# Performance work log

Hardware: AMD Instinct MI355X
Metric: run time of the kernel (lower is better)

## Reference

```python
import jax, jax.numpy as jnp
import numpy as np

B, N, H, HID, LOCALITY = 2, 4096, 4, 256, 30.0
VD = HID // H
F32_MAX = jnp.finfo(jnp.float32).max


def setup_inputs() -> dict:
    key = jax.random.key(0)
    k1, k2, k3, k4 = jax.random.split(key, 4)
    m_dist = jax.random.uniform(k1, (B, N, N), dtype=jnp.float32)  # pairwise distances (b,N,N)
    x = jax.random.normal(k2, (B, N, HID), dtype=jnp.float32)
    r = jax.random.normal(k3, (1, H, 1, 1), dtype=jnp.float32)  # learned per-head distance scale
    # lecun_normal: std = 1/sqrt(fan_in), fan_in = HID
    weight = jax.random.normal(k4, (H, HID, VD), dtype=jnp.float32) / np.sqrt(HID)
    return {"m_dist": m_dist, "x": x, "r": r, "weight": weight}


def reference(m_dist, x, r, weight):
    # scaled distance per head: (b,h,n,n)
    scaled = m_dist[:, None, :, :] * (r ** 2)
    # percentile-thresholded local mask (linear interpolation, per row)
    thresh = jnp.percentile(scaled, LOCALITY, axis=-1, keepdims=True, method="linear")
    scaled = jnp.where(scaled <= thresh, scaled, F32_MAX)
    att = jax.nn.softmax(-scaled, axis=-1)  # (b,h,n,n)
    value = jnp.einsum("bnj,hjk->bhnk", x, weight)  # (b,h,n,v)
    out = jnp.einsum("bhnj,bhjd->bhnd", att, value)  # (b,h,n,v)
    out = jnp.transpose(out, (0, 2, 1, 3)).reshape(out.shape[0], -1, HID)  # (b,n,hid)
    return jax.nn.gelu(out, approximate=False)
```

## Files before the change

kernel.cpp:

```cpp
#include <hip/hip_runtime.h>
#include <hip/hip_bf16.h>

#define Bc   2
#define Nc   4096
#define Hc   4
#define HIDc 256
#define VDc  64

typedef short s8v  __attribute__((ext_vector_type(8)));
typedef float f4v  __attribute__((ext_vector_type(4)));

static __device__ __forceinline__ unsigned short bf16bits(float f) {
    __hip_bfloat16 h = __float2bfloat16(f);
    return *(unsigned short*)&h;
}

__global__ __launch_bounds__(256) void front_kernel(
    const float* __restrict__ m_dist, const float* __restrict__ wgt,
    unsigned short* __restrict__ wh, unsigned short* __restrict__ wl,
    float* __restrict__ thr_out, float* __restrict__ min_out)
{
    int t = threadIdx.x, bid = blockIdx.x;

    if (bid < 128) {
        int h  = bid >> 5;
        int kt = (bid >> 3) & 3;
        int jc = bid & 7;
        int lane = t >> 2, ii = t & 3;
        #pragma unroll
        for (int u = 0; u < 2; u++) {
            int i = ii * 2 + u;
            int j = jc * 32 + (lane >> 4) * 8 + i;
            int k = kt * 16 + (lane & 15);
            float v = wgt[((size_t)h * HIDc + j) * VDc + k];
            __hip_bfloat16 hb = __float2bfloat16(v);
            float hf = __bfloat162float(hb);
            size_t o = ((((size_t)h * 4 + kt) * 8 + jc) * 64 + lane) * 8 + i;
            wh[o] = *(unsigned short*)&hb;
            wl[o] = bf16bits(v - hf);
        }
        return;
    }

    __shared__ unsigned int hist[1024];
    __shared__ float wredf[4];
    __shared__ unsigned int wsum[4];
    __shared__ unsigned int wscan[4];
    __shared__ int b0s, b1s;
    __shared__ unsigned int c0s;
    __shared__ unsigned int ncand;
    __shared__ float cand[256];
    __shared__ float s0s, s1s;

    size_t rowid = bid - 128;
    const float* row = m_dist + rowid * Nc;

    float4 vals[4];
    float lmin = 1e30f;
    #pragma unroll
    for (int i = 0; i < 4; i++) {
        float4 v = ((const float4*)row)[t + i * 256];
        vals[i] = v;
        lmin = fminf(lmin, fminf(fminf(v.x, v.y), fminf(v.z, v.w)));
    }
    #pragma unroll
    for (int o = 32; o > 0; o >>= 1) lmin = fminf(lmin, __shfl_xor(lmin, o));
    if ((t & 63) == 0) wredf[t >> 6] = lmin;

    const unsigned int R0 = 1228u, R1 = 1229u;
    float wlo = 0.25f, whi = 0.35f;
    int b0 = 0, b1 = 0;
    unsigned int C0 = 0;

    for (;;) {
        float wscale = 1024.0f / (whi - wlo);

        for (int i = t; i < 1024; i += 256) hist[i] = 0u;
        if (t == 0) ncand = 0u;
        __syncthreads();

        unsigned int cb = 0;
        #pragma unroll
        for (int i = 0; i < 4; i++) {
            float a[4] = {vals[i].x, vals[i].y, vals[i].z, vals[i].w};
            #pragma unroll
            for (int j = 0; j < 4; j++) {
                float v = a[j];
                if (v < wlo) {
                    cb++;
                } else {
                    int bx = (int)((v - wlo) * wscale);
                    if (bx < 1024) atomicAdd(&hist[bx], 1u);
                }
            }
        }
        #pragma unroll
        for (int o = 32; o > 0; o >>= 1) cb += __shfl_xor(cb, o);
        if ((t & 63) == 0) wsum[t >> 6] = cb;
        __syncthreads();
        unsigned int Cb = wsum[0] + wsum[1] + wsum[2] + wsum[3];

        unsigned int c[4], csum = 0;
        #pragma unroll
        for (int j = 0; j < 4; j++) { c[j] = hist[t * 4 + j]; csum += c[j]; }
        unsigned int inc = csum;
        #pragma unroll
        for (int o = 1; o < 64; o <<= 1) {
            unsigned int nv = __shfl_up(inc, o);
            if ((t & 63) >= o) inc += nv;
        }
        if ((t & 63) == 63) wscan[t >> 6] = inc;
        __syncthreads();
        unsigned int wpref = 0;
        for (int wv = 0; wv < (t >> 6); wv++) wpref += wscan[wv];
        unsigned int T = wscan[0] + wscan[1] + wscan[2] + wscan[3];
        unsigned int P = Cb + wpref + inc - csum;

        unsigned int cum = P;
        #pragma unroll
        for (int j = 0; j < 4; j++) {
            unsigned int lo = cum, hi = cum + c[j];
            if (R0 >= lo && R0 < hi) { b0s = t * 4 + j; c0s = lo; }
            if (R1 >= lo && R1 < hi) { b1s = t * 4 + j; }
            cum = hi;
        }
        __syncthreads();

        if (Cb <= R0 && R1 < Cb + T) { b0 = b0s; b1 = b1s; C0 = c0s; break; }
        wlo = 0.0f; whi = 1.001f;
    }

    float wscale = 1024.0f / (whi - wlo);
    #pragma unroll
    for (int i = 0; i < 4; i++) {
        float a[4] = {vals[i].x, vals[i].y, vals[i].z, vals[i].w};
        #pragma unroll
        for (int j = 0; j < 4; j++) {
            float v = a[j];
            if (v >= wlo) {
                int bx = (int)((v - wlo) * wscale);
                if (bx >= b0 && bx <= b1) {
                    unsigned int p = atomicAdd(&ncand, 1u);
                    if (p < 256u) cand[p] = v;
                }
            }
        }
    }
    __syncthreads();
    unsigned int nc = min(ncand, 256u);
    if ((unsigned int)t < nc) {
        float v = cand[t];
        unsigned int rk = C0;
        for (unsigned int j = 0; j < nc; j++) {
            float u = cand[j];
            rk += (u < v || (u == v && j < (unsigned int)t)) ? 1u : 0u;
        }
        if (rk == R0) s0s = v;
        if (rk == R1) s1s = v;
    }
    __syncthreads();
    if (t == 0) {
        thr_out[rowid] = 0.5f * (s0s + s1s);
        min_out[rowid] = fminf(fminf(wredf[0], wredf[1]), fminf(wredf[2], wredf[3]));
    }
}

__global__ __launch_bounds__(256) void value_kernel(
    const float* __restrict__ x,
    const unsigned short* __restrict__ wh, const unsigned short* __restrict__ wl,
    unsigned short* __restrict__ vt_g)
{
    int t  = threadIdx.x;
    int bid = blockIdx.x;
    int nt = bid & 63;
    int h  = (bid >> 6) & 3;
    int b  = bid >> 8;
    int n0 = nt * 64;

    int w = t >> 6, lane = t & 63, q4 = lane >> 4, m16 = lane & 15;
    int nb = n0 + w * 16;

    const float* xp = x + ((size_t)(b * Nc + nb + m16)) * HIDc + q4 * 8;

    f4v acc[4];
    #pragma unroll
    for (int kt = 0; kt < 4; kt++) acc[kt] = (f4v){0.f, 0.f, 0.f, 0.f};

    #pragma unroll
    for (int jc = 0; jc < 8; jc++) {
        float4 xv0 = *(const float4*)(xp + jc * 32);
        float4 xv1 = *(const float4*)(xp + jc * 32 + 4);
        float f[8] = {xv0.x, xv0.y, xv0.z, xv0.w, xv1.x, xv1.y, xv1.z, xv1.w};
        union { s8v v; unsigned short u[8]; } hs, ls;
        #pragma unroll
        for (int i = 0; i < 8; i++) {
            __hip_bfloat16 hb = __float2bfloat16(f[i]);
            float hf = __bfloat162float(hb);
            hs.u[i] = *(unsigned short*)&hb;
            ls.u[i] = bf16bits(f[i] - hf);
        }
        #pragma unroll
        for (int kt = 0; kt < 4; kt++) {
            size_t ao = (((size_t)(h * 4 + kt) * 8 + jc) << 9) + lane * 8;
            s8v ah = *(const s8v*)(wh + ao);
            s8v al = *(const s8v*)(wl + ao);
            acc[kt] = __builtin_amdgcn_mfma_f32_16x16x32_bf16(ah, hs.v, acc[kt], 0, 0, 0);
            acc[kt] = __builtin_amdgcn_mfma_f32_16x16x32_bf16(al, hs.v, acc[kt], 0, 0, 0);
            acc[kt] = __builtin_amdgcn_mfma_f32_16x16x32_bf16(ah, ls.v, acc[kt], 0, 0, 0);
        }
    }

    unsigned short* vg = vt_g + (((size_t)b * Hc + h) * VDc) * Nc;
    #pragma unroll
    for (int kt = 0; kt < 4; kt++) {
        #pragma unroll
        for (int rg = 0; rg < 4; rg++) {
            int k = kt * 16 + q4 * 4 + rg;
            vg[(size_t)k * Nc + nb + m16] = bf16bits(acc[kt][rg]);
        }
    }
}

#define NT 64
#define JT 64
#define BIGF 3.0e38f

__global__ __launch_bounds__(1024, 8) void attn_kernel(
    const float* __restrict__ m_dist, const float* __restrict__ rr,
    const unsigned short* __restrict__ vt_g,
    const float* __restrict__ thr_g, const float* __restrict__ min_g,
    float* __restrict__ Op, float* __restrict__ Zp, int jlen)
{
    __shared__ float ms[NT * 64];
    __shared__ unsigned short vt[Hc * VDc * 64];

    int t = threadIdx.x;
    const int nblk = Bc * (Nc / NT);
    int js = blockIdx.x / nblk;
    int rb = blockIdx.x - js * nblk;
    int b  = rb >> 6;
    int n0 = (rb & 63) * NT;
    int j0 = js * jlen;

    int lane = t & 63, q = lane >> 4, m16 = lane & 15;
    int w = t >> 6;
    int h = w & 3, rq = w >> 2;
    int row = rq * 16 + m16;

    float mn = min_g[b * Nc + n0 + row];
    float rv = rr[h];
    float cc = -(rv * rv) * 1.4426950408889634f;
    float nmncc = -mn * cc;

    f4v acc[4];
    #pragma unroll
    for (int ct = 0; ct < 4; ct++) acc[ct] = (f4v){0.f, 0.f, 0.f, 0.f};
    float zacc = 0.f;

    const float* mbase = m_dist + ((size_t)b * Nc + n0) * Nc + j0;
    const unsigned short* vtb = vt_g + ((size_t)b * Hc * VDc) * Nc + j0;

    int mrow = t >> 4, mch = t & 15;
    int msw  = mrow * 64 + ((mch ^ (mrow & 15)) << 2);
    float thm = thr_g[b * Nc + n0 + mrow];

    int schunk8 = ((t & 7) ^ ((t >> 3) & 7)) * 8;
    unsigned short* vt_wbase = &vt[(w * 8) * 64];

    int a00 = row * 64 + (((q * 2 + 0) ^ m16) << 2);
    int a01 = row * 64 + (((q * 2 + 1) ^ m16) << 2);
    int a10 = row * 64 + (((8 + q * 2 + 0) ^ m16) << 2);
    int a11 = row * 64 + (((8 + q * 2 + 1) ^ m16) << 2);

    for (int jt = 0; jt < jlen; jt += JT) {
        #pragma unroll
        for (int i = 0; i < 2; i++) {
            int rrow = (t >> 3) + i * 128;
            __builtin_amdgcn_global_load_lds(
                (const __attribute__((address_space(1))) void*)
                    (vtb + (size_t)rrow * Nc + jt + schunk8),
                (__attribute__((address_space(3))) void*)
                    (vt_wbase + i * 128 * 64),
                16, 0, 0);
        }
        {
            float4 v = *(const float4*)(mbase + (size_t)mrow * Nc + jt + mch * 4);
            v.x = (v.x <= thm) ? v.x : BIGF;
            v.y = (v.y <= thm) ? v.y : BIGF;
            v.z = (v.z <= thm) ? v.z : BIGF;
            v.w = (v.w <= thm) ? v.w : BIGF;
            *(float4*)&ms[msw] = v;
        }
        __syncthreads();

        __builtin_amdgcn_s_setprio(1);
        const unsigned short* vb = &vt[(h * VDc) * 64];
        #pragma unroll
        for (int ks = 0; ks < 2; ks++) {
            float4 a0 = *(const float4*)&ms[ks ? a10 : a00];
            float4 a1 = *(const float4*)&ms[ks ? a11 : a01];
            float w0 = __builtin_amdgcn_exp2f(__builtin_fmaf(a0.x, cc, nmncc));
            float w1 = __builtin_amdgcn_exp2f(__builtin_fmaf(a0.y, cc, nmncc));
            float w2 = __builtin_amdgcn_exp2f(__builtin_fmaf(a0.z, cc, nmncc));
            float w3 = __builtin_amdgcn_exp2f(__builtin_fmaf(a0.w, cc, nmncc));
            float w4 = __builtin_amdgcn_exp2f(__builtin_fmaf(a1.x, cc, nmncc));
            float w5 = __builtin_amdgcn_exp2f(__builtin_fmaf(a1.y, cc, nmncc));
            float w6 = __builtin_amdgcn_exp2f(__builtin_fmaf(a1.z, cc, nmncc));
            float w7 = __builtin_amdgcn_exp2f(__builtin_fmaf(a1.w, cc, nmncc));
            zacc += ((w0 + w1) + (w2 + w3)) + ((w4 + w5) + (w6 + w7));
            union { s8v v; __hip_bfloat162 h2[4]; } afu;
            afu.h2[0] = __float22bfloat162_rn((float2){w0, w1});
            afu.h2[1] = __float22bfloat162_rn((float2){w2, w3});
            afu.h2[2] = __float22bfloat162_rn((float2){w4, w5});
            afu.h2[3] = __float22bfloat162_rn((float2){w6, w7});
            #pragma unroll
            for (int ct = 0; ct < 4; ct++) {
                int brow = ct * 16 + m16;
                s8v bf = *(const s8v*)(vb + brow * 64 + (((ks * 4 + q) ^ (m16 & 7)) << 3));
                acc[ct] = __builtin_amdgcn_mfma_f32_16x16x32_bf16(afu.v, bf, acc[ct], 0, 0, 0);
            }
        }
        __builtin_amdgcn_s_setprio(0);
        __syncthreads();
    }

    zacc += __shfl_xor(zacc, 16);
    zacc += __shfl_xor(zacc, 32);
    if (q == 0)
        Zp[(((size_t)js * Bc + b) * Hc + h) * Nc + n0 + row] = zacc;

    #pragma unroll
    for (int ct = 0; ct < 4; ct++) {
        #pragma unroll
        for (int rg = 0; rg < 4; rg++) {
            int nl = rq * 16 + q * 4 + rg;
            Op[(((size_t)js * Bc + b) * Nc + n0 + nl) * HIDc + h * VDc + ct * 16 + m16]
                = acc[ct][rg];
        }
    }
}

__global__ __launch_bounds__(256) void combine_kernel(
    const float* __restrict__ Op, const float* __restrict__ Zp,
    float* __restrict__ out, int S)
{
    int g = blockIdx.x * 256 + threadIdx.x;
    int c4 = g & 63;
    int n  = (g >> 6) & (Nc - 1);
    int b  = g >> 18;
    int h  = c4 >> 4;

    float z = 0.f;
    float4 v = {0.f, 0.f, 0.f, 0.f};
    for (int s = 0; s < S; s++) {
        z += Zp[(((size_t)s * Bc + b) * Hc + h) * Nc + n];
        float4 p = *(const float4*)&Op[(((size_t)s * Bc + b) * Nc + n) * HIDc + c4 * 4];
        v.x += p.x; v.y += p.y; v.z += p.z; v.w += p.w;
    }
    float iz = 1.0f / z;
    float4 o;
    float u;
    u = v.x * iz; o.x = 0.5f * u * (1.0f + erff(u * 0.7071067811865476f));
    u = v.y * iz; o.y = 0.5f * u * (1.0f + erff(u * 0.7071067811865476f));
    u = v.z * iz; o.z = 0.5f * u * (1.0f + erff(u * 0.7071067811865476f));
    u = v.w * iz; o.w = 0.5f * u * (1.0f + erff(u * 0.7071067811865476f));
    *(float4*)&out[(((size_t)b * Nc + n) * HIDc) + c4 * 4] = o;
}

extern "C" void kernel_launch(void* const* d_in, const int* in_sizes, int n_in,
                              void* d_out, int out_size, void* d_ws, size_t ws_size,
                              hipStream_t stream) {
    const float* m_dist = (const float*)d_in[0];
    const float* x      = (const float*)d_in[1];
    const float* r      = (const float*)d_in[2];
    const float* weight = (const float*)d_in[3];
    float* out = (float*)d_out;

    char* ws = (char*)d_ws;
    const size_t MB = 1024 * 1024;
    unsigned short* vt = (unsigned short*)ws;
    float* thr = (float*)(ws + 4 * MB);
    float* mn  = (float*)(ws + 4 * MB + 32 * 1024);
    float* Zp  = (float*)(ws + 4 * MB + 64 * 1024);
    float* Op  = (float*)(ws + 5 * MB);

    const size_t OpSz = (size_t)Bc * Nc * HIDc * 4;
    int S = 4;
    if (ws_size < 6 * MB + 4 * OpSz) S = 2;
    if (ws_size < 6 * MB + 2 * OpSz) S = 1;
    int jlen = Nc / S;

    char* pb = ws + 5 * MB + (size_t)S * OpSz;
    unsigned short* wh = (unsigned short*)pb;
    unsigned short* wl = (unsigned short*)(pb + 128 * 1024);

    front_kernel<<<128 + Bc * Nc, 256, 0, stream>>>(m_dist, weight, wh, wl, thr, mn);
    value_kernel<<<512, 256, 0, stream>>>(x, wh, wl, vt);
    attn_kernel<<<S * Bc * (Nc / NT), 1024, 0, stream>>>(m_dist, r, vt, thr, mn, Op, Zp, jlen);
    combine_kernel<<<(Bc * Nc * HIDc) / 1024, 256, 0, stream>>>(Op, Zp, out, S);
}
```

Measured before the change: 266.4 us.

## Double-buffer attention j-tiles with register prefetch and halve JT

```diff
diff --git a/kernel.cpp b/kernel.cpp
--- a/kernel.cpp
+++ b/kernel.cpp
@@ -222,7 +222,7 @@
 }
 
 #define NT 64
-#define JT 64
+#define JT 32
 #define BIGF 3.0e38f
 
 __global__ __launch_bounds__(1024, 8) void attn_kernel(
@@ -231,8 +231,8 @@
     const float* __restrict__ thr_g, const float* __restrict__ min_g,
     float* __restrict__ Op, float* __restrict__ Zp, int jlen)
 {
-    __shared__ float ms[NT * 64];
-    __shared__ unsigned short vt[Hc * VDc * 64];
+    __shared__ float ms[2][NT * JT];
+    __shared__ unsigned short vt[2][Hc * VDc * JT];
 
     int t = threadIdx.x;
     const int nblk = Bc * (Nc / NT);
@@ -260,68 +260,74 @@
     const float* mbase = m_dist + ((size_t)b * Nc + n0) * Nc + j0;
     const unsigned short* vtb = vt_g + ((size_t)b * Hc * VDc) * Nc + j0;
 
-    int mrow = t >> 4, mch = t & 15;
-    int msw  = mrow * 64 + ((mch ^ (mrow & 15)) << 2);
-    float thm = thr_g[b * Nc + n0 + mrow];
-
-    int schunk8 = ((t & 7) ^ ((t >> 3) & 7)) * 8;
-    unsigned short* vt_wbase = &vt[(w * 8) * 64];
-
-    int a00 = row * 64 + (((q * 2 + 0) ^ m16) << 2);
-    int a01 = row * 64 + (((q * 2 + 1) ^ m16) << 2);
-    int a10 = row * 64 + (((8 + q * 2 + 0) ^ m16) << 2);
-    int a11 = row * 64 + (((8 + q * 2 + 1) ^ m16) << 2);
-
-    for (int jt = 0; jt < jlen; jt += JT) {
-        #pragma unroll
-        for (int i = 0; i < 2; i++) {
-            int rrow = (t >> 3) + i * 128;
-            __builtin_amdgcn_global_load_lds(
-                (const __attribute__((address_space(1))) void*)
-                    (vtb + (size_t)rrow * Nc + jt + schunk8),
-                (__attribute__((address_space(3))) void*)
-                    (vt_wbase + i * 128 * 64),
-                16, 0, 0);
-        }
-        {
-            float4 v = *(const float4*)(mbase + (size_t)mrow * Nc + jt + mch * 4);
+    int mrow = t >> 3, mch = t & 7;
+    int msw  = mrow * JT + ((mch ^ (mrow & 7)) << 2);
+    const float* msrc = mbase + (size_t)mrow * Nc + mch * 4;
+    float thm = (t < 512) ? thr_g[b * Nc + n0 + mrow] : 0.f;
+
+    int vrow = t >> 2;
+    int vlc  = (t & 3) ^ (vrow & 3);
+    const unsigned short* vsrc = vtb + (size_t)vrow * Nc + vlc * 8;
+
+    int s7 = m16 & 7;
+    int a0o = row * JT + (((q * 2 + 0) ^ s7) << 2);
+    int a1o = row * JT + (((q * 2 + 1) ^ s7) << 2);
+    int bco = (q ^ (m16 & 3)) << 3;
+
+    int niter = jlen / JT;
+
+    float4 msreg;
+    if (t < 512) msreg = *(const float4*)(msrc);
+    __builtin_amdgcn_global_load_lds(
+        (const __attribute__((address_space(1))) void*)(vsrc),
+        (__attribute__((address_space(3))) void*)(&vt[0][(size_t)t * 8]),
+        16, 0, 0);
+
+    int cur = 0;
+    for (int it = 0; it < niter; ++it) {
+        if (t < 512) {
+            float4 v = msreg;
             v.x = (v.x <= thm) ? v.x : BIGF;
             v.y = (v.y <= thm) ? v.y : BIGF;
             v.z = (v.z <= thm) ? v.z : BIGF;
             v.w = (v.w <= thm) ? v.w : BIGF;
-            *(float4*)&ms[msw] = v;
+            *(float4*)&ms[cur][msw] = v;
         }
         __syncthreads();
 
-        __builtin_amdgcn_s_setprio(1);
-        const unsigned short* vb = &vt[(h * VDc) * 64];
-        #pragma unroll
-        for (int ks = 0; ks < 2; ks++) {
-            float4 a0 = *(const float4*)&ms[ks ? a10 : a00];
-            float4 a1 = *(const float4*)&ms[ks ? a11 : a01];
-            float w0 = __builtin_amdgcn_exp2f(__builtin_fmaf(a0.x, cc, nmncc));
-            float w1 = __builtin_amdgcn_exp2f(__builtin_fmaf(a0.y, cc, nmncc));
-            float w2 = __builtin_amdgcn_exp2f(__builtin_fmaf(a0.z, cc, nmncc));
-            float w3 = __builtin_amdgcn_exp2f(__builtin_fmaf(a0.w, cc, nmncc));
-            float w4 = __builtin_amdgcn_exp2f(__builtin_fmaf(a1.x, cc, nmncc));
-            float w5 = __builtin_amdgcn_exp2f(__builtin_fmaf(a1.y, cc, nmncc));
-            float w6 = __builtin_amdgcn_exp2f(__builtin_fmaf(a1.z, cc, nmncc));
-            float w7 = __builtin_amdgcn_exp2f(__builtin_fmaf(a1.w, cc, nmncc));
-            zacc += ((w0 + w1) + (w2 + w3)) + ((w4 + w5) + (w6 + w7));
-            union { s8v v; __hip_bfloat162 h2[4]; } afu;
-            afu.h2[0] = __float22bfloat162_rn((float2){w0, w1});
-            afu.h2[1] = __float22bfloat162_rn((float2){w2, w3});
-            afu.h2[2] = __float22bfloat162_rn((float2){w4, w5});
-            afu.h2[3] = __float22bfloat162_rn((float2){w6, w7});
-            #pragma unroll
-            for (int ct = 0; ct < 4; ct++) {
-                int brow = ct * 16 + m16;
-                s8v bf = *(const s8v*)(vb + brow * 64 + (((ks * 4 + q) ^ (m16 & 7)) << 3));
-                acc[ct] = __builtin_amdgcn_mfma_f32_16x16x32_bf16(afu.v, bf, acc[ct], 0, 0, 0);
-            }
-        }
-        __builtin_amdgcn_s_setprio(0);
-        __syncthreads();
+        if (it + 1 < niter) {
+            int jn = (it + 1) * JT;
+            if (t < 512) msreg = *(const float4*)(msrc + jn);
+            __builtin_amdgcn_global_load_lds(
+                (const __attribute__((address_space(1))) void*)(vsrc + jn),
+                (__attribute__((address_space(3))) void*)(&vt[cur ^ 1][(size_t)t * 8]),
+                16, 0, 0);
+        }
+
+        const unsigned short* vb = &vt[cur][h * VDc * JT];
+        float4 a0 = *(const float4*)&ms[cur][a0o];
+        float4 a1 = *(const float4*)&ms[cur][a1o];
+        float w0 = __builtin_amdgcn_exp2f(__builtin_fmaf(a0.x, cc, nmncc));
+        float w1 = __builtin_amdgcn_exp2f(__builtin_fmaf(a0.y, cc, nmncc));
+        float w2 = __builtin_amdgcn_exp2f(__builtin_fmaf(a0.z, cc, nmncc));
+        float w3 = __builtin_amdgcn_exp2f(__builtin_fmaf(a0.w, cc, nmncc));
+        float w4 = __builtin_amdgcn_exp2f(__builtin_fmaf(a1.x, cc, nmncc));
+        float w5 = __builtin_amdgcn_exp2f(__builtin_fmaf(a1.y, cc, nmncc));
+        float w6 = __builtin_amdgcn_exp2f(__builtin_fmaf(a1.z, cc, nmncc));
+        float w7 = __builtin_amdgcn_exp2f(__builtin_fmaf(a1.w, cc, nmncc));
+        zacc += ((w0 + w1) + (w2 + w3)) + ((w4 + w5) + (w6 + w7));
+        union { s8v v; __hip_bfloat162 h2[4]; } afu;
+        afu.h2[0] = __float22bfloat162_rn((float2){w0, w1});
+        afu.h2[1] = __float22bfloat162_rn((float2){w2, w3});
+        afu.h2[2] = __float22bfloat162_rn((float2){w4, w5});
+        afu.h2[3] = __float22bfloat162_rn((float2){w6, w7});
+        #pragma unroll
+        for (int ct = 0; ct < 4; ct++) {
+            int brow = ct * 16 + m16;
+            s8v bf = *(const s8v*)(vb + brow * JT + bco);
+            acc[ct] = __builtin_amdgcn_mfma_f32_16x16x32_bf16(afu.v, bf, acc[ct], 0, 0, 0);
+        }
+        cur ^= 1;
     }
 
     zacc += __shfl_xor(zacc, 16);
```

After: 263.1 us (median of 2 runs). Within noise of the previous version (-1.2%).

## Restructure attention kernel into LDS-free per-wave tiles covering all heads

Applied to the files above, without the earlier changes.

```diff
diff --git a/kernel.cpp b/kernel.cpp
--- a/kernel.cpp
+++ b/kernel.cpp
@@ -221,121 +221,101 @@
     }
 }
 
-#define NT 64
-#define JT 64
-#define BIGF 3.0e38f
-
-__global__ __launch_bounds__(1024, 8) void attn_kernel(
+#define JT 32
+
+__global__ __launch_bounds__(128, 4) void attn_kernel(
     const float* __restrict__ m_dist, const float* __restrict__ rr,
     const unsigned short* __restrict__ vt_g,
     const float* __restrict__ thr_g, const float* __restrict__ min_g,
     float* __restrict__ Op, float* __restrict__ Zp, int jlen)
 {
-    __shared__ float ms[NT * 64];
-    __shared__ unsigned short vt[Hc * VDc * 64];
+    int nwg = (int)gridDim.x;
+    int cpx = nwg >> 3;
+    int bid = ((int)blockIdx.x & 7) * cpx + ((int)blockIdx.x >> 3);
+
+    const int tpj = Bc * (Nc / 32);
+    int js = bid / tpj;
+    int rb = bid - js * tpj;
+    int b  = rb >> 7;
+    int n0 = (rb & 127) * 32;
+    int j0 = js * jlen;
 
     int t = threadIdx.x;
-    const int nblk = Bc * (Nc / NT);
-    int js = blockIdx.x / nblk;
-    int rb = blockIdx.x - js * nblk;
-    int b  = rb >> 6;
-    int n0 = (rb & 63) * NT;
-    int j0 = js * jlen;
-
     int lane = t & 63, q = lane >> 4, m16 = lane & 15;
     int w = t >> 6;
-    int h = w & 3, rq = w >> 2;
-    int row = rq * 16 + m16;
-
-    float mn = min_g[b * Nc + n0 + row];
-    float rv = rr[h];
-    float cc = -(rv * rv) * 1.4426950408889634f;
-    float nmncc = -mn * cc;
-
-    f4v acc[4];
-    #pragma unroll
-    for (int ct = 0; ct < 4; ct++) acc[ct] = (f4v){0.f, 0.f, 0.f, 0.f};
-    float zacc = 0.f;
-
-    const float* mbase = m_dist + ((size_t)b * Nc + n0) * Nc + j0;
-    const unsigned short* vtb = vt_g + ((size_t)b * Hc * VDc) * Nc + j0;
-
-    int mrow = t >> 4, mch = t & 15;
-    int msw  = mrow * 64 + ((mch ^ (mrow & 15)) << 2);
-    float thm = thr_g[b * Nc + n0 + mrow];
-
-    int schunk8 = ((t & 7) ^ ((t >> 3) & 7)) * 8;
-    unsigned short* vt_wbase = &vt[(w * 8) * 64];
-
-    int a00 = row * 64 + (((q * 2 + 0) ^ m16) << 2);
-    int a01 = row * 64 + (((q * 2 + 1) ^ m16) << 2);
-    int a10 = row * 64 + (((8 + q * 2 + 0) ^ m16) << 2);
-    int a11 = row * 64 + (((8 + q * 2 + 1) ^ m16) << 2);
+    int row = n0 + w * 16 + m16;
+
+    float mn  = min_g[b * Nc + row];
+    float thm = thr_g[b * Nc + row];
+    float cch[4], nmh[4];
+    #pragma unroll
+    for (int h = 0; h < 4; h++) {
+        float rv = rr[h];
+        cch[h] = -(rv * rv) * 1.4426950408889634f;
+        nmh[h] = -mn * cch[h];
+    }
+
+    f4v acc[4][4];
+    #pragma unroll
+    for (int h = 0; h < 4; h++)
+        #pragma unroll
+        for (int ct = 0; ct < 4; ct++) acc[h][ct] = (f4v){0.f, 0.f, 0.f, 0.f};
+    float z[4] = {0.f, 0.f, 0.f, 0.f};
+
+    const float* mrow = m_dist + ((size_t)b * Nc + row) * Nc + j0 + q * 8;
+    const unsigned short* vtb = vt_g + ((size_t)b * Hc * VDc) * Nc + j0 + q * 8;
+    int voffh[4];
+    #pragma unroll
+    for (int h = 0; h < 4; h++) voffh[h] = (h * VDc + m16) * Nc;
 
     for (int jt = 0; jt < jlen; jt += JT) {
-        #pragma unroll
-        for (int i = 0; i < 2; i++) {
-            int rrow = (t >> 3) + i * 128;
-            __builtin_amdgcn_global_load_lds(
-                (const __attribute__((address_space(1))) void*)
-                    (vtb + (size_t)rrow * Nc + jt + schunk8),
-                (__attribute__((address_space(3))) void*)
-                    (vt_wbase + i * 128 * 64),
-                16, 0, 0);
-        }
-        {
-            float4 v = *(const float4*)(mbase + (size_t)mrow * Nc + jt + mch * 4);
-            v.x = (v.x <= thm) ? v.x : BIGF;
-            v.y = (v.y <= thm) ? v.y : BIGF;
-            v.z = (v.z <= thm) ? v.z : BIGF;
-            v.w = (v.w <= thm) ? v.w : BIGF;
-            *(float4*)&ms[msw] = v;
-        }
-        __syncthreads();
-
-        __builtin_amdgcn_s_setprio(1);
-        const unsigned short* vb = &vt[(h * VDc) * 64];
-        #pragma unroll
-        for (int ks = 0; ks < 2; ks++) {
-            float4 a0 = *(const float4*)&ms[ks ? a10 : a00];
-            float4 a1 = *(const float4*)&ms[ks ? a11 : a01];
-            float w0 = __builtin_amdgcn_exp2f(__builtin_fmaf(a0.x, cc, nmncc));
-            float w1 = __builtin_amdgcn_exp2f(__builtin_fmaf(a0.y, cc, nmncc));
-            float w2 = __builtin_amdgcn_exp2f(__builtin_fmaf(a0.z, cc, nmncc));
-            float w3 = __builtin_amdgcn_exp2f(__builtin_fmaf(a0.w, cc, nmncc));
-            float w4 = __builtin_amdgcn_exp2f(__builtin_fmaf(a1.x, cc, nmncc));
-            float w5 = __builtin_amdgcn_exp2f(__builtin_fmaf(a1.y, cc, nmncc));
-            float w6 = __builtin_amdgcn_exp2f(__builtin_fmaf(a1.z, cc, nmncc));
-            float w7 = __builtin_amdgcn_exp2f(__builtin_fmaf(a1.w, cc, nmncc));
-            zacc += ((w0 + w1) + (w2 + w3)) + ((w4 + w5) + (w6 + w7));
-            union { s8v v; __hip_bfloat162 h2[4]; } afu;
-            afu.h2[0] = __float22bfloat162_rn((float2){w0, w1});
-            afu.h2[1] = __float22bfloat162_rn((float2){w2, w3});
-            afu.h2[2] = __float22bfloat162_rn((float2){w4, w5});
-            afu.h2[3] = __float22bfloat162_rn((float2){w6, w7});
+        float4 d0 = *(const float4*)(mrow + jt);
+        float4 d1 = *(const float4*)(mrow + jt + 4);
+        #pragma unroll
+        for (int h = 0; h < 4; h++) {
+            float cc = cch[h], nm = nmh[h];
+            float w0 = (d0.x <= thm) ? __builtin_amdgcn_exp2f(__builtin_fmaf(d0.x, cc, nm)) : 0.f;
+            float w1 = (d0.y <= thm) ? __builtin_amdgcn_exp2f(__builtin_fmaf(d0.y, cc, nm)) : 0.f;
+            float w2 = (d0.z <= thm) ? __builtin_amdgcn_exp2f(__builtin_fmaf(d0.z, cc, nm)) : 0.f;
+            float w3 = (d0.w <= thm) ? __builtin_amdgcn_exp2f(__builtin_fmaf(d0.w, cc, nm)) : 0.f;
+            float w4 = (d1.x <= thm) ? __builtin_amdgcn_exp2f(__builtin_fmaf(d1.x, cc, nm)) : 0.f;
+            float w5 = (d1.y <= thm) ? __builtin_amdgcn_exp2f(__builtin_fmaf(d1.y, cc, nm)) : 0.f;
+            float w6 = (d1.z <= thm) ? __builtin_amdgcn_exp2f(__builtin_fmaf(d1.z, cc, nm)) : 0.f;
+            float w7 = (d1.w <= thm) ? __builtin_amdgcn_exp2f(__builtin_fmaf(d1.w, cc, nm)) : 0.f;
+            z[h] += ((w0 + w1) + (w2 + w3)) + ((w4 + w5) + (w6 + w7));
+            union { s8v v; __hip_bfloat162 h2[4]; } af;
+            af.h2[0] = __float22bfloat162_rn((float2){w0, w1});
+            af.h2[1] = __float22bfloat162_rn((float2){w2, w3});
+            af.h2[2] = __float22bfloat162_rn((float2){w4, w5});
+            af.h2[3] = __float22bfloat162_rn((float2){w6, w7});
+            const unsigned short* vjb = vtb + jt + voffh[h];
             #pragma unroll
             for (int ct = 0; ct < 4; ct++) {
-                int brow = ct * 16 + m16;
-                s8v bf = *(const s8v*)(vb + brow * 64 + (((ks * 4 + q) ^ (m16 & 7)) << 3));
-                acc[ct] = __builtin_amdgcn_mfma_f32_16x16x32_bf16(afu.v, bf, acc[ct], 0, 0, 0);
+                s8v bf = *(const s8v*)(vjb + ct * (16 * Nc));
+                acc[h][ct] = __builtin_amdgcn_mfma_f32_16x16x32_bf16(af.v, bf, acc[h][ct], 0, 0, 0);
             }
         }
-        __builtin_amdgcn_s_setprio(0);
-        __syncthreads();
-    }
-
-    zacc += __shfl_xor(zacc, 16);
-    zacc += __shfl_xor(zacc, 32);
-    if (q == 0)
-        Zp[(((size_t)js * Bc + b) * Hc + h) * Nc + n0 + row] = zacc;
-
-    #pragma unroll
-    for (int ct = 0; ct < 4; ct++) {
-        #pragma unroll
-        for (int rg = 0; rg < 4; rg++) {
-            int nl = rq * 16 + q * 4 + rg;
-            Op[(((size_t)js * Bc + b) * Nc + n0 + nl) * HIDc + h * VDc + ct * 16 + m16]
-                = acc[ct][rg];
+    }
+
+    #pragma unroll
+    for (int h = 0; h < 4; h++) {
+        float zz = z[h];
+        zz += __shfl_xor(zz, 16);
+        zz += __shfl_xor(zz, 32);
+        if (q == 0)
+            Zp[(((size_t)js * Bc + b) * Hc + h) * Nc + row] = zz;
+    }
+
+    #pragma unroll
+    for (int h = 0; h < 4; h++) {
+        #pragma unroll
+        for (int ct = 0; ct < 4; ct++) {
+            #pragma unroll
+            for (int rg = 0; rg < 4; rg++) {
+                int nl = n0 + w * 16 + q * 4 + rg;
+                Op[(((size_t)js * Bc + b) * Nc + nl) * HIDc + h * VDc + ct * 16 + m16]
+                    = acc[h][ct][rg];
+            }
         }
     }
 }
@@ -382,20 +362,21 @@
     float* thr = (float*)(ws + 4 * MB);
     float* mn  = (float*)(ws + 4 * MB + 32 * 1024);
     float* Zp  = (float*)(ws + 4 * MB + 64 * 1024);
-    float* Op  = (float*)(ws + 5 * MB);
+    float* Op  = (float*)(ws + 6 * MB);
 
     const size_t OpSz = (size_t)Bc * Nc * HIDc * 4;
-    int S = 4;
-    if (ws_size < 6 * MB + 4 * OpSz) S = 2;
-    if (ws_size < 6 * MB + 2 * OpSz) S = 1;
+    int S = 8;
+    if (ws_size < 7 * MB + 8 * OpSz) S = 4;
+    if (ws_size < 7 * MB + 4 * OpSz) S = 2;
+    if (ws_size < 7 * MB + 2 * OpSz) S = 1;
     int jlen = Nc / S;
 
-    char* pb = ws + 5 * MB + (size_t)S * OpSz;
+    char* pb = ws + 6 * MB + (size_t)S * OpSz;
     unsigned short* wh = (unsigned short*)pb;
     unsigned short* wl = (unsigned short*)(pb + 128 * 1024);
 
     front_kernel<<<128 + Bc * Nc, 256, 0, stream>>>(m_dist, weight, wh, wl, thr, mn);
     value_kernel<<<512, 256, 0, stream>>>(x, wh, wl, vt);
-    attn_kernel<<<S * Bc * (Nc / NT), 1024, 0, stream>>>(m_dist, r, vt, thr, mn, Op, Zp, jlen);
+    attn_kernel<<<S * Bc * (Nc / 32), 128, 0, stream>>>(m_dist, r, vt, thr, mn, Op, Zp, jlen);
     combine_kernel<<<(Bc * Nc * HIDc) / 1024, 256, 0, stream>>>(Op, Zp, out, S);
 }
```

Result: slower. 361.1 us (+35.5%).
